# Kernel tuning notes

Measured on AMD Instinct MI355X. Metric: run time of the kernel, lower is better.

Reference implementation:

```python
import jax, jax.numpy as jnp
import numpy as np


def setup_inputs() -> dict:
    key = jax.random.key(0)
    B, N, M, D = 8, 256, 16, 256
    embeddings = jax.random.normal(key, (B, N, M, D), dtype=jnp.float32)
    w = jnp.asarray(10.0, dtype=jnp.float32)
    b = jnp.asarray(-5.0, dtype=jnp.float32)
    return {"embeddings": embeddings, "w": w, "b": b}


def reference(embeddings, w, b):
    # embeddings: [B, N, M, D]
    B, N, M, D = embeddings.shape
    centroids = jnp.mean(embeddings, axis=2)  # [B, N, D]

    # Cross similarities: S[b,j,i,k] = w * <e_{bji}, c_{bk}> + b
    S = w * jnp.einsum('bjid,bkd->bjik', embeddings, centroids) + b  # [B,N,M,N]

    # Own-centroid case (j == k): leave-one-out centroid
    # <e, (M*c_j - e)/(M-1)> = (M*<e,c_j> - ||e||^2) / (M-1)
    dot_own = jnp.einsum('bjid,bjd->bji', embeddings, centroids)     # [B,N,M]
    sq_norm = jnp.sum(embeddings * embeddings, axis=-1)              # [B,N,M]
    S_self = w * (M * dot_own - sq_norm) / (M - 1) + b               # [B,N,M]

    # Place S_self on the k == j diagonal
    eye = jnp.eye(N, dtype=bool)[None, :, None, :]                   # [1,N,1,N]
    S = jnp.where(eye, S_self[..., None], S)

    # loss = sum log sum_k exp(S) - sum_{j==k} S
    loss = jnp.sum(jax.nn.logsumexp(S, axis=-1)) - jnp.sum(S_self)
    return loss
```

## Files before the change

### kernel.cpp

```cpp
#include <hip/hip_runtime.h>

constexpr int B = 8, N = 256, M = 16, D = 256;

typedef short bf16x8 __attribute__((ext_vector_type(8)));
typedef float f32x4 __attribute__((ext_vector_type(4)));

__device__ __forceinline__ unsigned short f2bf(float x) {
  unsigned u = __float_as_uint(x);
  u = (u + 0x7FFFu + ((u >> 16) & 1u)) >> 16;
  return (unsigned short)u;
}
__device__ __forceinline__ uint4 packbf8(const float* f) {
  uint4 u;
  u.x = (unsigned)f2bf(f[0]) | ((unsigned)f2bf(f[1]) << 16);
  u.y = (unsigned)f2bf(f[2]) | ((unsigned)f2bf(f[3]) << 16);
  u.z = (unsigned)f2bf(f[4]) | ((unsigned)f2bf(f[5]) << 16);
  u.w = (unsigned)f2bf(f[6]) | ((unsigned)f2bf(f[7]) << 16);
  return u;
}


__global__ __launch_bounds__(256) void k_prep(const float* __restrict__ e,
                                              uint4* __restrict__ EbfA,
                                              uint4* __restrict__ Cbf,
                                              float* __restrict__ SQ,
                                              float* __restrict__ out) {
  const int blk = blockIdx.x;
  const int b = blk >> 8, j = blk & 255;
  const int t = threadIdx.x;
  const int w = t >> 6, l = t & 63;
  const int m = l & 15, q = l >> 4;
  const float* base = e + (size_t)blk * (M * D);

  float sqp = 0.f;
  __shared__ float sqred[4][16];

#pragma unroll
  for (int kk = 0; kk < 2; ++kk) {
    const int kc = w * 2 + kk;
    const float* src = base + m * D + kc * 32 + q * 8;
    float f[8];
#pragma unroll
    for (int x = 0; x < 4; ++x) f[x] = ((const float4*)src)->x, f[x] = src[x];
#pragma unroll
    for (int x = 0; x < 8; ++x) f[x] = src[x];
    EbfA[(size_t)(blk * 8 + kc) * 64 + l] = packbf8(f);
#pragma unroll
    for (int x = 0; x < 8; ++x) sqp = fmaf(f[x], f[x], sqp);
    float cv[8];
#pragma unroll
    for (int x = 0; x < 8; ++x) cv[x] = f[x];
#pragma unroll
    for (int mk = 1; mk < 16; mk <<= 1)
#pragma unroll
      for (int x = 0; x < 8; ++x) cv[x] += __shfl_xor(cv[x], mk, 64);
    if (m == (j & 15)) {
      float cs[8];
#pragma unroll
      for (int x = 0; x < 8; ++x) cs[x] = cv[x] * (1.f / 16.f);
      Cbf[(size_t)((b * 8 + kc) * 16 + (j >> 4)) * 64 + l] = packbf8(cs);
    }
  }
  sqp += __shfl_xor(sqp, 16, 64);
  sqp += __shfl_xor(sqp, 32, 64);
  if (q == 0) sqred[w][m] = sqp;
  __syncthreads();
  if (t < 16) SQ[blk * 16 + t] = sqred[0][t] + sqred[1][t] + sqred[2][t] + sqred[3][t];
  if (blk == 0 && t == 0) out[0] = 0.f;
}

__global__ __launch_bounds__(256) void k_gemm(const uint4* __restrict__ EbfA,
                                              const uint4* __restrict__ Cbf,
                                              const float* __restrict__ SQ,
                                              const float* __restrict__ wp,
                                              const float* __restrict__ bp,
                                              float* __restrict__ out) {
  const int blk = blockIdx.x;
  const int b = blk >> 6, strip = blk & 63;
  const int tid = threadIdx.x;
  const int wid = tid >> 6, lane = tid & 63;
  const int h = wid >> 1, c = wid & 1;
  const int q = lane >> 4, cl_ = lane & 15;

  const uint4* Ab = EbfA + (size_t)((b * 256 + strip * 4 + h * 2) * 8) * 64 + lane;
  const uint4* Bb = Cbf + (size_t)(b * 128 + c * 8) * 64 + lane;

  f32x4 acc[2][8];
#pragma unroll
  for (int rt = 0; rt < 2; ++rt)
#pragma unroll
    for (int nt = 0; nt < 8; ++nt) acc[rt][nt] = (f32x4)0.f;

#pragma unroll 1
  for (int kc = 0; kc < 8; ++kc) {
    uint4 af0 = Ab[kc * 64];
    uint4 af1 = Ab[(8 + kc) * 64];
    uint4 bfr[8];
#pragma unroll
    for (int nt = 0; nt < 8; ++nt) bfr[nt] = Bb[(kc * 16 + nt) * 64];
    bf16x8 a0 = __builtin_bit_cast(bf16x8, af0);
    bf16x8 a1 = __builtin_bit_cast(bf16x8, af1);
#pragma unroll
    for (int nt = 0; nt < 8; ++nt) {
      bf16x8 bv = __builtin_bit_cast(bf16x8, bfr[nt]);
      acc[0][nt] = __builtin_amdgcn_mfma_f32_16x16x32_bf16(a0, bv, acc[0][nt], 0, 0, 0);
      acc[1][nt] = __builtin_amdgcn_mfma_f32_16x16x32_bf16(a1, bv, acc[1][nt], 0, 0, 0);
    }
  }

  const float w = *wp, bias = *bp;
  __shared__ float lmx[2][64];
  __shared__ float lsm[2][64];
  __shared__ float bred[4];
  float ssum = 0.f;

#pragma unroll
  for (int rt = 0; rt < 2; ++rt) {
    const int jr = strip * 4 + h * 2 + rt;
    const bool own = (c == (jr >> 7)) && (cl_ == (jr & 15));
    const int ntd = (jr >> 4) & 7;
    float sq[4];
    if (own) {
#pragma unroll
      for (int reg = 0; reg < 4; ++reg)
        sq[reg] = SQ[b * 4096 + strip * 64 + (h * 2 + rt) * 16 + q * 4 + reg];
    }
#pragma unroll
    for (int nt = 0; nt < 8; ++nt)
#pragma unroll
      for (int reg = 0; reg < 4; ++reg) {
        const float raw = acc[rt][nt][reg];
        float sv = fmaf(w, raw, bias);
        if (own && nt == ntd) {
          sv = fmaf(w * (1.f / 15.f), 16.f * raw - sq[reg], bias);
          ssum += sv;
        }
        acc[rt][nt][reg] = sv;
      }
#pragma unroll
    for (int reg = 0; reg < 4; ++reg) {
      float mx = acc[rt][0][reg];
#pragma unroll
      for (int nt = 1; nt < 8; ++nt) mx = fmaxf(mx, acc[rt][nt][reg]);
#pragma unroll
      for (int mk = 1; mk < 16; mk <<= 1) mx = fmaxf(mx, __shfl_xor(mx, mk, 64));
      if (cl_ == 0) lmx[c][(h * 2 + rt) * 16 + q * 4 + reg] = mx;
    }
  }
  __syncthreads();

#pragma unroll
  for (int rt = 0; rt < 2; ++rt)
#pragma unroll
    for (int reg = 0; reg < 4; ++reg) {
      const int Rl = (h * 2 + rt) * 16 + q * 4 + reg;
      const float mx = fmaxf(lmx[0][Rl], lmx[1][Rl]);
      float se = 0.f;
#pragma unroll
      for (int nt = 0; nt < 8; ++nt) se += __expf(acc[rt][nt][reg] - mx);
#pragma unroll
      for (int mk = 1; mk < 16; mk <<= 1) se += __shfl_xor(se, mk, 64);
      if (cl_ == 0) lsm[c][Rl] = se;
    }
  __syncthreads();

  float part = -ssum;
  if (c == 0 && cl_ == 0) {
#pragma unroll
    for (int rt = 0; rt < 2; ++rt)
#pragma unroll
      for (int reg = 0; reg < 4; ++reg) {
        const int Rl = (h * 2 + rt) * 16 + q * 4 + reg;
        const float mx = fmaxf(lmx[0][Rl], lmx[1][Rl]);
        part += mx + __logf(lsm[0][Rl] + lsm[1][Rl]);
      }
  }
#pragma unroll
  for (int mk = 1; mk < 64; mk <<= 1) part += __shfl_xor(part, mk, 64);
  if (lane == 0) bred[wid] = part;
  __syncthreads();
  if (tid == 0) atomicAdd(out, bred[0] + bred[1] + bred[2] + bred[3]);
}

extern "C" void kernel_launch(void* const* d_in, const int* in_sizes, int n_in,
                              void* d_out, int out_size, void* d_ws, size_t ws_size,
                              hipStream_t stream) {
  const float* e = (const float*)d_in[0];
  const float* wp = (const float*)d_in[1];
  const float* bp = (const float*)d_in[2];
  float* out = (float*)d_out;
  char* ws = (char*)d_ws;
  uint4* EbfA = (uint4*)ws;
  uint4* Cbf = (uint4*)(ws + (size_t)16 * 1024 * 1024);
  float* SQ = (float*)(ws + (size_t)17 * 1024 * 1024);

  k_prep<<<B * N, 256, 0, stream>>>(e, EbfA, Cbf, SQ, out);
  k_gemm<<<B * 64, 256, 0, stream>>>(EbfA, Cbf, SQ, wp, bp, out);
}
```

Before: 97.53 us.

## Vectorize prep loads and compute centroids via column sums in shared memory

```diff
diff --git a/kernel.cpp b/kernel.cpp
--- a/kernel.cpp
+++ b/kernel.cpp
@@ -28,43 +28,43 @@
   const int blk = blockIdx.x;
   const int b = blk >> 8, j = blk & 255;
   const int t = threadIdx.x;
-  const int w = t >> 6, l = t & 63;
-  const int m = l & 15, q = l >> 4;
   const float* base = e + (size_t)blk * (M * D);
 
-  float sqp = 0.f;
+  __shared__ float cbuf[D];
   __shared__ float sqred[4][16];
 
+  float cs = 0.f;
 #pragma unroll
-  for (int kk = 0; kk < 2; ++kk) {
-    const int kc = w * 2 + kk;
-    const float* src = base + m * D + kc * 32 + q * 8;
-    float f[8];
+  for (int i = 0; i < M; ++i) cs += base[i * D + t];
+  cbuf[t] = cs * (1.f / 16.f);
+
+  const int m = t & 15, o2 = t >> 4;
+  const float* p0 = base + m * D + o2 * 8;
+  float f0[8], f1[8];
+  *(float4*)(f0) = *(const float4*)(p0);
+  *(float4*)(f0 + 4) = *(const float4*)(p0 + 4);
+  *(float4*)(f1) = *(const float4*)(p0 + 128);
+  *(float4*)(f1 + 4) = *(const float4*)(p0 + 132);
+
+  EbfA[(size_t)(blk * 8 + (o2 >> 2)) * 64 + (o2 & 3) * 16 + m] = packbf8(f0);
+  EbfA[(size_t)(blk * 8 + 4 + (o2 >> 2)) * 64 + (o2 & 3) * 16 + m] = packbf8(f1);
+
+  float sqp = 0.f;
 #pragma unroll
-    for (int x = 0; x < 4; ++x) f[x] = ((const float4*)src)->x, f[x] = src[x];
-#pragma unroll
-    for (int x = 0; x < 8; ++x) f[x] = src[x];
-    EbfA[(size_t)(blk * 8 + kc) * 64 + l] = packbf8(f);
-#pragma unroll
-    for (int x = 0; x < 8; ++x) sqp = fmaf(f[x], f[x], sqp);
-    float cv[8];
-#pragma unroll
-    for (int x = 0; x < 8; ++x) cv[x] = f[x];
-#pragma unroll
-    for (int mk = 1; mk < 16; mk <<= 1)
-#pragma unroll
-      for (int x = 0; x < 8; ++x) cv[x] += __shfl_xor(cv[x], mk, 64);
-    if (m == (j & 15)) {
-      float cs[8];
-#pragma unroll
-      for (int x = 0; x < 8; ++x) cs[x] = cv[x] * (1.f / 16.f);
-      Cbf[(size_t)((b * 8 + kc) * 16 + (j >> 4)) * 64 + l] = packbf8(cs);
-    }
-  }
+  for (int x = 0; x < 8; ++x) sqp = fmaf(f0[x], f0[x], fmaf(f1[x], f1[x], sqp));
   sqp += __shfl_xor(sqp, 16, 64);
   sqp += __shfl_xor(sqp, 32, 64);
-  if (q == 0) sqred[w][m] = sqp;
+  const int w = t >> 6;
+  if ((t & 63) < 16) sqred[w][m] = sqp;
   __syncthreads();
+
+  if (t < 32) {
+    float cf[8];
+#pragma unroll
+    for (int x = 0; x < 8; ++x) cf[x] = cbuf[t * 8 + x];
+    Cbf[((size_t)(b * 8 + (t >> 2)) * 16 + (j >> 4)) * 64 + (t & 3) * 16 + (j & 15)] =
+        packbf8(cf);
+  }
   if (t < 16) SQ[blk * 16 + t] = sqred[0][t] + sqred[1][t] + sqred[2][t] + sqred[3][t];
   if (blk == 0 && t == 0) out[0] = 0.f;
 }
```

New measurement: 97.36 us (median of 2 runs). About the same (-0.2%).
